# Optimization experiments

Measured on AMD Instinct MI355X. Metric: run time of the kernel, lower is better.

The kernel has to match this reference:

```python
import jax, jax.numpy as jnp
import numpy as np

B, N, E, H = 64, 512, 1024, 16
DH = E // H


def setup_inputs() -> dict:
    key = jax.random.key(0)
    ks = jax.random.split(key, 5)
    x = jax.random.normal(ks[0], (B, N, E), dtype=jnp.float32)
    # Linear weights stored as [in, out] (transpose of torch's [out, in]); y = x @ W + b
    Wqkv = jax.random.normal(ks[1], (E, 3 * E), dtype=jnp.float32) * 0.02
    bqkv = jnp.zeros((3 * E,), dtype=jnp.float32)
    Wproj = jax.random.normal(ks[2], (E, E), dtype=jnp.float32) * 0.02
    bproj = jnp.zeros((E,), dtype=jnp.float32)
    adj = jax.random.randint(ks[3], (N, N), 0, 2, dtype=jnp.int32)
    return {"x": x, "Wqkv": Wqkv, "bqkv": bqkv, "Wproj": Wproj, "bproj": bproj, "adj": adj}


def reference(x, Wqkv, bqkv, Wproj, bproj, adj):
    b, n, e = x.shape
    h, dh = H, e // H
    # fused QKV projection
    qkv = (x @ Wqkv + bqkv).reshape(b, n, 3, h, dh)
    qkv = jnp.transpose(qkv, (2, 0, 3, 1, 4))  # [3, B, H, N, Dh]
    q, k, v = qkv[0], qkv[1], qkv[2]
    # adjacency mask with self-loops (adj + eye, then bool), broadcast over B, H
    mask = (adj + jnp.eye(n, dtype=adj.dtype)) > 0  # [N, N]
    scale = 1.0 / jnp.sqrt(jnp.asarray(dh, dtype=x.dtype))
    scores = jnp.einsum("bhnd,bhmd->bhnm", q, k) * scale  # [B, H, N, N]
    scores = jnp.where(mask[None, None], scores, jnp.finfo(scores.dtype).min)
    attn = jax.nn.softmax(scores, axis=-1)
    y = jnp.einsum("bhnm,bhmd->bhnd", attn, v)  # [B, H, N, Dh]
    y = jnp.transpose(y, (0, 2, 1, 3)).reshape(b, n, e)
    return y @ Wproj + bproj
```

## Files before the change

### kernel.cpp

```cpp
#include <hip/hip_runtime.h>
#include <hip/hip_bf16.h>

#define Bz 64
#define Nz 512
#define Ez 1024
#define Hz 16
#define DHz 64

static constexpr int MROWS = Bz * Nz;
static constexpr int NQKV  = 3 * Ez;

typedef __attribute__((ext_vector_type(8))) short bf16x8_t;
typedef __attribute__((ext_vector_type(4))) float f32x4_t;
typedef __attribute__((ext_vector_type(16))) float f32x16_t;
typedef __attribute__((ext_vector_type(4))) unsigned u32x4_t;

union FragU { bf16x8_t h; u32x4_t u; };

__device__ __forceinline__ unsigned short f2bf(float f) {
    union { float f; unsigned u; } v; v.f = f;
    unsigned r = v.u + 0x7FFFu + ((v.u >> 16) & 1u);
    return (unsigned short)(r >> 16);
}
__device__ __forceinline__ float bf2f(unsigned short h) {
    union { unsigned u; float f; } v; v.u = ((unsigned)h) << 16;
    return v.f;
}
__device__ __forceinline__ unsigned packbf(float a, float b) {
    union { float f; unsigned u; } x, y; x.f = a; y.f = b;
    return ((x.u + 0x8000u) >> 16) | ((y.u + 0x8000u) & 0xFFFF0000u);
}

__device__ __forceinline__ void async16(const unsigned short* g, unsigned short* l) {
    __builtin_amdgcn_global_load_lds(
        (const __attribute__((address_space(1))) void*)g,
        (__attribute__((address_space(3))) void*)l, 16, 0, 0);
}

__device__ __forceinline__ void barrier_lds() {
    asm volatile("s_waitcnt lgkmcnt(0)" ::: "memory");
    __builtin_amdgcn_sched_barrier(0);
    __builtin_amdgcn_s_barrier();
    __builtin_amdgcn_sched_barrier(0);
}

__global__ void cvt_f32_bf16(const float* __restrict__ in,
                             unsigned short* __restrict__ out, int n4) {
    int id = blockIdx.x * blockDim.x + threadIdx.x;
    int stride = gridDim.x * blockDim.x;
    for (int i = id; i < n4; i += stride) {
        float4 f = ((const float4*)in)[i];
        ushort4 o;
        o.x = f2bf(f.x); o.y = f2bf(f.y); o.z = f2bf(f.z); o.w = f2bf(f.w);
        ((ushort4*)out)[i] = o;
    }
}

__global__ __launch_bounds__(256)
void cvt_transpose(const float* __restrict__ in,
                   unsigned short* __restrict__ out,
                   int K, int Ncols) {
    int n  = blockIdx.x * 256 + threadIdx.x;
    int k0 = blockIdx.y * 8;
    bf16x8_t o;
#pragma unroll
    for (int j = 0; j < 8; j++)
        o[j] = (short)f2bf(in[(long)(k0 + j) * Ncols + n]);
    *(bf16x8_t*)&out[(long)n * K + k0] = o;
}

__global__ void build_adjm(const int* __restrict__ adj,
                           unsigned long long* __restrict__ adjm) {
    int id = blockIdx.x * blockDim.x + threadIdx.x;
    int n = id >> 3, w = id & 7;
    const int4* r4 = (const int4*)(adj + (long)n * Nz + w * 64);
    unsigned long long m = 0;
#pragma unroll
    for (int c = 0; c < 16; c++) {
        int4 v = r4[c];
        unsigned long long bits =
            (unsigned long long)(v.x != 0) | ((unsigned long long)(v.y != 0) << 1) |
            ((unsigned long long)(v.z != 0) << 2) | ((unsigned long long)(v.w != 0) << 3);
        m |= bits << (c * 4);
    }
    if ((n >> 6) == w) m |= 1ull << (n & 63);
    adjm[id] = m;
}

template<bool OUT_BF16>
__global__ __launch_bounds__(512, 2)
void gemm_mfma(const unsigned short* __restrict__ A,
               const unsigned short* __restrict__ BT,
               const float* __restrict__ bias,
               void* __restrict__ C,
               int M, int Ncols, int K) {
    const int tid  = threadIdx.x;
    const int w    = tid >> 6;
    const int lane = tid & 63;
    const int m32  = lane & 31;
    const int kh   = lane >> 5;
    const int wm   = (w >> 2) * 128;
    const int wn   = (w & 3) * 64;

    const int nwg = gridDim.x * gridDim.y;
    const int bid = blockIdx.y * gridDim.x + blockIdx.x;
    const int swz = (bid & 7) * (nwg >> 3) + (bid >> 3);
    const int rowBase = (swz / gridDim.x) * 256;
    const int colBase = (swz % gridDim.x) * 256;

    __shared__ __align__(16) unsigned short Abuf[2][256][64];
    __shared__ __align__(16) unsigned short Bbuf[2][256][64];

    f32x16_t acc[4][2];
#pragma unroll
    for (int mi = 0; mi < 4; mi++)
#pragma unroll
        for (int n = 0; n < 2; n++)
#pragma unroll
            for (int r = 0; r < 16; r++)
                acc[mi][n][r] = 0.0f;

    const unsigned short* srcA[4];
    const unsigned short* srcB[4];
#pragma unroll
    for (int li = 0; li < 4; li++) {
        int s = (w * 4 + li) * 64 + lane;
        int r = s >> 3;
        int c = (s & 7) ^ (r & 7);
        srcA[li] = A  + (size_t)(rowBase + r) * K + c * 8;
        srcB[li] = BT + (size_t)(colBase + r) * K + c * 8;
    }
    const int dstOff = w * 2048;

    const int nt = K >> 6;
    const int fsw = m32 & 7;

#pragma unroll
    for (int li = 0; li < 4; li++)
        async16(srcA[li], (unsigned short*)Abuf[0] + dstOff + li * 512);
#pragma unroll
    for (int li = 0; li < 4; li++)
        async16(srcB[li], (unsigned short*)Bbuf[0] + dstOff + li * 512);
#pragma unroll
    for (int li = 0; li < 4; li++)
        async16(srcB[li] + 64, (unsigned short*)Bbuf[1] + dstOff + li * 512);
    asm volatile("s_waitcnt vmcnt(4)" ::: "memory");
    __builtin_amdgcn_sched_barrier(0);
    __builtin_amdgcn_s_barrier();
    __builtin_amdgcn_sched_barrier(0);

    for (int t = 0; t < nt; t++) {
        const int buf = t & 1;
        bf16x8_t af[2][4], bfr[2][4];

        if (t + 1 < nt) {
#pragma unroll
            for (int li = 0; li < 4; li++)
                async16(srcA[li] + (t + 1) * 64,
                        (unsigned short*)Abuf[buf ^ 1] + dstOff + li * 512);
        }
#pragma unroll
        for (int kc = 0; kc < 4; kc++) {
            int p = (kc * 2 + kh) ^ fsw;
#pragma unroll
            for (int n = 0; n < 2; n++)
                bfr[n][kc] = *(const bf16x8_t*)&Bbuf[buf][wn + n * 32 + m32][p * 8];
#pragma unroll
            for (int mi = 0; mi < 2; mi++)
                af[mi][kc] = *(const bf16x8_t*)&Abuf[buf][wm + mi * 32 + m32][p * 8];
        }
        __builtin_amdgcn_s_setprio(1);
#pragma unroll
        for (int kc = 0; kc < 4; kc++)
#pragma unroll
            for (int mi = 0; mi < 2; mi++)
#pragma unroll
                for (int n = 0; n < 2; n++)
                    acc[mi][n] = __builtin_amdgcn_mfma_f32_32x32x16_bf16(
                        af[mi][kc], bfr[n][kc], acc[mi][n], 0, 0, 0);
        __builtin_amdgcn_s_setprio(0);
        barrier_lds();

        if (t + 2 < nt) {
#pragma unroll
            for (int li = 0; li < 4; li++)
                async16(srcB[li] + (t + 2) * 64,
                        (unsigned short*)Bbuf[buf] + dstOff + li * 512);
        }
#pragma unroll
        for (int kc = 0; kc < 4; kc++) {
            int p = (kc * 2 + kh) ^ fsw;
#pragma unroll
            for (int mi = 0; mi < 2; mi++)
                af[mi][kc] = *(const bf16x8_t*)&Abuf[buf][wm + 64 + mi * 32 + m32][p * 8];
        }
        __builtin_amdgcn_s_setprio(1);
#pragma unroll
        for (int kc = 0; kc < 4; kc++)
#pragma unroll
            for (int mi = 0; mi < 2; mi++)
#pragma unroll
                for (int n = 0; n < 2; n++)
                    acc[2 + mi][n] = __builtin_amdgcn_mfma_f32_32x32x16_bf16(
                        af[mi][kc], bfr[n][kc], acc[2 + mi][n], 0, 0, 0);
        __builtin_amdgcn_s_setprio(0);

        if (t + 2 < nt) {
            asm volatile("s_waitcnt vmcnt(4)" ::: "memory");
            barrier_lds();
        } else if (t + 1 < nt) {
            asm volatile("s_waitcnt vmcnt(0)" ::: "memory");
            barrier_lds();
        }
    }

#pragma unroll
    for (int n = 0; n < 2; n++) {
        int col = colBase + wn + n * 32 + m32;
        float bv = bias[col];
#pragma unroll
        for (int mi = 0; mi < 4; mi++) {
#pragma unroll
            for (int reg = 0; reg < 16; reg++) {
                int row = rowBase + wm + mi * 32 + (reg & 3) + 8 * (reg >> 2) + 4 * kh;
                float v = acc[mi][n][reg] + bv;
                if (OUT_BF16)
                    ((unsigned short*)C)[(size_t)row * Ncols + col] = f2bf(v);
                else
                    ((float*)C)[(size_t)row * Ncols + col] = v;
            }
        }
    }
}

__global__ __launch_bounds__(512, 2)
void attn_mfma(const unsigned short* __restrict__ qkv,
               const unsigned long long* __restrict__ adjm,
               unsigned short* __restrict__ y)
{
    const int h = blockIdx.x;
    const int b = blockIdx.y;
    const int tid  = threadIdx.x;
    const int lane = tid & 63;
    const int w    = tid >> 6;
    const int l16  = lane & 15;
    const int q    = lane >> 4;

    __shared__ __align__(16) unsigned short Ks[512][64];
    __shared__ __align__(16) unsigned short Vt[64][512];

    const long rowB = (long)b * Nz;
    const unsigned short* base = qkv + rowB * NQKV;

    for (int idx = tid; idx < 4096; idx += 512) {
        int n = idx >> 3, cc = idx & 7;
        *(bf16x8_t*)&Ks[n][(cc ^ (n & 7)) * 8] =
            *(const bf16x8_t*)&base[(long)n * NQKV + Ez + h * DHz + cc * 8];
    }
    {
        int tp = tid & 255, dh = tid >> 8;
        int n0 = tp * 2;
        bf16x8_t va[4], vb[4];
#pragma unroll
        for (int c = 0; c < 4; c++) {
            va[c] = *(const bf16x8_t*)&base[(long)n0 * NQKV + 2 * Ez + h * DHz + dh * 32 + c * 8];
            vb[c] = *(const bf16x8_t*)&base[(long)(n0 + 1) * NQKV + 2 * Ez + h * DHz + dh * 32 + c * 8];
        }
        unsigned short* vt = &Vt[0][0];
#pragma unroll
        for (int dd = 0; dd < 32; dd++) {
            int d = dh * 32 + dd;
            unsigned lo = (unsigned)(unsigned short)va[dd >> 3][dd & 7];
            unsigned hi = (unsigned)(unsigned short)vb[dd >> 3][dd & 7];
            int cp = (n0 >> 3) ^ (d & 7);
            *(unsigned*)&vt[d * 512 + cp * 8 + (n0 & 7)] = lo | (hi << 16);
        }
    }
    FragU qf[4][2];
#pragma unroll
    for (int mt = 0; mt < 4; mt++)
#pragma unroll
        for (int kc = 0; kc < 2; kc++)
            qf[mt][kc].h = *(const bf16x8_t*)&base[(long)(w * 64 + mt * 16 + l16) * NQKV
                                                   + h * DHz + kc * 32 + q * 8];
    __syncthreads();

    f32x4_t oacc[4][4];
#pragma unroll
    for (int mt = 0; mt < 4; mt++)
#pragma unroll
        for (int dt = 0; dt < 4; dt++) {
            f32x4_t z = {0.0f, 0.0f, 0.0f, 0.0f};
            oacc[mt][dt] = z;
        }
    float rsum[4] = {0.0f, 0.0f, 0.0f, 0.0f};
    unsigned long long wm[4];

    for (int ct = 0; ct < 16; ct++) {
        const int j0 = ct * 32;
        if ((ct & 1) == 0) {
#pragma unroll
            for (int mt = 0; mt < 4; mt++)
                wm[mt] = adjm[(size_t)(w * 64 + mt * 16 + l16) * 8 + (ct >> 1)];
        }
        bf16x8_t kf[2][2];
#pragma unroll
        for (int jt = 0; jt < 2; jt++)
#pragma unroll
            for (int kc = 0; kc < 2; kc++)
                kf[jt][kc] = *(const bf16x8_t*)
                    &Ks[j0 + jt * 16 + l16][((kc * 4 + q) ^ (l16 & 7)) * 8];

        f32x4_t tacc[2][4];
#pragma unroll
        for (int jt = 0; jt < 2; jt++)
#pragma unroll
            for (int mt = 0; mt < 4; mt++) {
                f32x4_t z = {0.0f, 0.0f, 0.0f, 0.0f};
                z = __builtin_amdgcn_mfma_f32_16x16x32_bf16(kf[jt][0], qf[mt][0].h, z, 0, 0, 0);
                tacc[jt][mt] = __builtin_amdgcn_mfma_f32_16x16x32_bf16(kf[jt][1], qf[mt][1].h, z, 0, 0, 0);
            }

        unsigned pk[2][4][2];
#pragma unroll
        for (int jt = 0; jt < 2; jt++)
#pragma unroll
            for (int mt = 0; mt < 4; mt++) {
                float e[4];
#pragma unroll
                for (int r = 0; r < 4; r++) {
                    int jrel = (ct & 1) * 32 + jt * 16 + q * 4 + r;
                    bool bit = (wm[mt] >> jrel) & 1ull;
                    float ev = bit ? __expf(tacc[jt][mt][r] * 0.125f) : 0.0f;
                    e[r] = ev;
                    rsum[mt] += ev;
                }
                pk[jt][mt][0] = packbf(e[0], e[1]);
                pk[jt][mt][1] = packbf(e[2], e[3]);
            }

        bf16x8_t vf[4];
#pragma unroll
        for (int dt = 0; dt < 4; dt++) {
            int d = dt * 16 + l16;
            int cp = (ct * 4 + q) ^ (l16 & 7);
            vf[dt] = *(const bf16x8_t*)&(&Vt[0][0])[d * 512 + cp * 8];
        }

#pragma unroll
        for (int mt = 0; mt < 4; mt++) {
            FragU pf;
#pragma unroll
            for (int p = 0; p < 4; p++) {
                int srcl = ((lane & 16) << 1) | ((p & 2) << 3) | l16;
                unsigned a0 = (unsigned)__shfl((int)pk[0][mt][p & 1], srcl);
                unsigned a1 = (unsigned)__shfl((int)pk[1][mt][p & 1], srcl);
                pf.u[p] = (lane & 32) ? a1 : a0;
            }
#pragma unroll
            for (int dt = 0; dt < 4; dt++)
                oacc[mt][dt] = __builtin_amdgcn_mfma_f32_16x16x32_bf16(
                    pf.h, vf[dt], oacc[mt][dt], 0, 0, 0);
        }
    }

#pragma unroll
    for (int mt = 0; mt < 4; mt++) {
        float s = rsum[mt];
        s += __shfl_xor(s, 16);
        s += __shfl_xor(s, 32);
#pragma unroll
        for (int r = 0; r < 4; r++) {
            float rs = __shfl(s, (lane & 48) | (q * 4) | r);
            float inv = 1.0f / rs;
            int row = w * 64 + mt * 16 + q * 4 + r;
#pragma unroll
            for (int dt = 0; dt < 4; dt++)
                y[(rowB + row) * Ez + h * DHz + dt * 16 + l16] =
                    f2bf(oacc[mt][dt][r] * inv);
        }
    }
}

extern "C" void kernel_launch(void* const* d_in, const int* in_sizes, int n_in,
                              void* d_out, int out_size, void* d_ws, size_t ws_size,
                              hipStream_t stream) {
    const float* x     = (const float*)d_in[0];
    const float* Wqkv  = (const float*)d_in[1];
    const float* bqkv  = (const float*)d_in[2];
    const float* Wproj = (const float*)d_in[3];
    const float* bproj = (const float*)d_in[4];
    const int*   adj   = (const int*)d_in[5];
    float* out = (float*)d_out;

    char* ws = (char*)d_ws;
    unsigned short* xb     = (unsigned short*)(ws);
    unsigned short* qkv    = (unsigned short*)(ws + 67108864);
    unsigned short* WqkvT  = (unsigned short*)(ws + 268435456);
    unsigned short* WprojT = (unsigned short*)(ws + 274726912);
    unsigned long long* adjm = (unsigned long long*)(ws + 276824064);
    unsigned short* yb = xb;

    cvt_f32_bf16<<<8192, 256, 0, stream>>>(x, xb, (Bz * Nz * Ez) / 4);
    cvt_transpose<<<dim3(NQKV / 256, Ez / 8), 256, 0, stream>>>(Wqkv, WqkvT, Ez, NQKV);
    cvt_transpose<<<dim3(Ez / 256, Ez / 8), 256, 0, stream>>>(Wproj, WprojT, Ez, Ez);
    build_adjm<<<16, 256, 0, stream>>>(adj, adjm);

    gemm_mfma<true><<<dim3(NQKV / 256, MROWS / 256), 512, 0, stream>>>(
        xb, WqkvT, bqkv, qkv, MROWS, NQKV, Ez);

    attn_mfma<<<dim3(Hz, Bz), 512, 0, stream>>>(qkv, adjm, yb);

    gemm_mfma<false><<<dim3(Ez / 256, MROWS / 256), 512, 0, stream>>>(
        yb, WprojT, bproj, out, MROWS, Ez, Ez);
}
```

Measured before the change: 753.5 us.

## Restructure GEMM main loop into four half-K phases with finer async staging

Splits each 64-wide K tile of the bf16 GEMM into two 32-wide halves stored in separate LDS buffers, packing two logical rows per 64-element LDS row with a new XOR swizzle. The main loop becomes four phases, each issuing one async global-to-LDS stage, reading fragments and running eight MFMAs between barriers. The aim is to spread global loads more evenly across the iteration and keep more loads in flight, hiding memory latency behind MFMA work. In exchange it adds more barriers per tile and intricate vmcnt bookkeeping that must match the load count exactly.

```diff
diff --git a/kernel.cpp b/kernel.cpp
--- a/kernel.cpp
+++ b/kernel.cpp
@@ -37,12 +37,7 @@
         (__attribute__((address_space(3))) void*)l, 16, 0, 0);
 }
 
-__device__ __forceinline__ void barrier_lds() {
-    asm volatile("s_waitcnt lgkmcnt(0)" ::: "memory");
-    __builtin_amdgcn_sched_barrier(0);
-    __builtin_amdgcn_s_barrier();
-    __builtin_amdgcn_sched_barrier(0);
-}
+#define MFMA32(a, b, c) __builtin_amdgcn_mfma_f32_32x32x16_bf16(a, b, c, 0, 0, 0)
 
 __global__ void cvt_f32_bf16(const float* __restrict__ in,
                              unsigned short* __restrict__ out, int n4) {
@@ -108,8 +103,8 @@
     const int rowBase = (swz / gridDim.x) * 256;
     const int colBase = (swz % gridDim.x) * 256;
 
-    __shared__ __align__(16) unsigned short Abuf[2][256][64];
-    __shared__ __align__(16) unsigned short Bbuf[2][256][64];
+    __shared__ __align__(16) unsigned short Ah[2][2][128][64];
+    __shared__ __align__(16) unsigned short Bh[2][2][128][64];
 
     f32x16_t acc[4][2];
 #pragma unroll
@@ -120,99 +115,112 @@
             for (int r = 0; r < 16; r++)
                 acc[mi][n][r] = 0.0f;
 
-    const unsigned short* srcA[4];
-    const unsigned short* srcB[4];
-#pragma unroll
-    for (int li = 0; li < 4; li++) {
-        int s = (w * 4 + li) * 64 + lane;
-        int r = s >> 3;
-        int c = (s & 7) ^ (r & 7);
-        srcA[li] = A  + (size_t)(rowBase + r) * K + c * 8;
-        srcB[li] = BT + (size_t)(colBase + r) * K + c * 8;
-    }
-    const int dstOff = w * 2048;
+    const unsigned short* sA[2];
+    const unsigned short* sB[2];
+#pragma unroll
+    for (int l = 0; l < 2; l++) {
+        int s = l * 512 + tid;
+        int R = s >> 3, g = s & 7;
+        int lg = g ^ (R & 7);
+        int grow = 2 * R + (lg >> 2);
+        int gc8 = (lg & 3) * 8;
+        sA[l] = A  + (size_t)(rowBase + grow) * K + gc8;
+        sB[l] = BT + (size_t)(colBase + grow) * K + gc8;
+    }
+    const int dst0 = w * 512;
+
+#define STAGE(src, dst, tt, half) do {                                   \
+        unsigned short* d_ = &(dst)[0][0];                               \
+        async16((src)[0] + (size_t)(tt) * 64 + (half) * 32, d_ + dst0);  \
+        async16((src)[1] + (size_t)(tt) * 64 + (half) * 32, d_ + 4096 + dst0); \
+    } while (0)
+
+    const int Ra  = wm / 2 + (m32 >> 1);
+    const int Rb  = wn / 2 + (m32 >> 1);
+    const int key = (m32 >> 1) & 7;
+    const int lgb = (m32 & 1) * 4 + kh;
 
     const int nt = K >> 6;
-    const int fsw = m32 & 7;
-
-#pragma unroll
-    for (int li = 0; li < 4; li++)
-        async16(srcA[li], (unsigned short*)Abuf[0] + dstOff + li * 512);
-#pragma unroll
-    for (int li = 0; li < 4; li++)
-        async16(srcB[li], (unsigned short*)Bbuf[0] + dstOff + li * 512);
-#pragma unroll
-    for (int li = 0; li < 4; li++)
-        async16(srcB[li] + 64, (unsigned short*)Bbuf[1] + dstOff + li * 512);
-    asm volatile("s_waitcnt vmcnt(4)" ::: "memory");
+
+    STAGE(sA, Ah[0][0], 0, 0);
+    STAGE(sB, Bh[0][0], 0, 0);
+    STAGE(sA, Ah[0][1], 0, 1);
+    STAGE(sB, Bh[0][1], 0, 1);
+    STAGE(sA, Ah[1][0], 1, 0);
+    STAGE(sB, Bh[1][0], 1, 0);
+    asm volatile("s_waitcnt vmcnt(8)" ::: "memory");
     __builtin_amdgcn_sched_barrier(0);
     __builtin_amdgcn_s_barrier();
     __builtin_amdgcn_sched_barrier(0);
 
-    for (int t = 0; t < nt; t++) {
+    for (int t = 0; t < nt; ++t) {
         const int buf = t & 1;
-        bf16x8_t af[2][4], bfr[2][4];
-
-        if (t + 1 < nt) {
-#pragma unroll
-            for (int li = 0; li < 4; li++)
-                async16(srcA[li] + (t + 1) * 64,
-                        (unsigned short*)Abuf[buf ^ 1] + dstOff + li * 512);
-        }
-#pragma unroll
-        for (int kc = 0; kc < 4; kc++) {
-            int p = (kc * 2 + kh) ^ fsw;
-#pragma unroll
-            for (int n = 0; n < 2; n++)
-                bfr[n][kc] = *(const bf16x8_t*)&Bbuf[buf][wn + n * 32 + m32][p * 8];
-#pragma unroll
-            for (int mi = 0; mi < 2; mi++)
-                af[mi][kc] = *(const bf16x8_t*)&Abuf[buf][wm + mi * 32 + m32][p * 8];
-        }
-        __builtin_amdgcn_s_setprio(1);
-#pragma unroll
-        for (int kc = 0; kc < 4; kc++)
-#pragma unroll
-            for (int mi = 0; mi < 2; mi++)
-#pragma unroll
-                for (int n = 0; n < 2; n++)
-                    acc[mi][n] = __builtin_amdgcn_mfma_f32_32x32x16_bf16(
-                        af[mi][kc], bfr[n][kc], acc[mi][n], 0, 0, 0);
-        __builtin_amdgcn_s_setprio(0);
-        barrier_lds();
-
-        if (t + 2 < nt) {
-#pragma unroll
-            for (int li = 0; li < 4; li++)
-                async16(srcB[li] + (t + 2) * 64,
-                        (unsigned short*)Bbuf[buf] + dstOff + li * 512);
-        }
-#pragma unroll
-        for (int kc = 0; kc < 4; kc++) {
-            int p = (kc * 2 + kh) ^ fsw;
-#pragma unroll
-            for (int mi = 0; mi < 2; mi++)
-                af[mi][kc] = *(const bf16x8_t*)&Abuf[buf][wm + 64 + mi * 32 + m32][p * 8];
-        }
-        __builtin_amdgcn_s_setprio(1);
-#pragma unroll
-        for (int kc = 0; kc < 4; kc++)
-#pragma unroll
-            for (int mi = 0; mi < 2; mi++)
-#pragma unroll
-                for (int n = 0; n < 2; n++)
-                    acc[2 + mi][n] = __builtin_amdgcn_mfma_f32_32x32x16_bf16(
-                        af[mi][kc], bfr[n][kc], acc[2 + mi][n], 0, 0, 0);
-        __builtin_amdgcn_s_setprio(0);
-
-        if (t + 2 < nt) {
-            asm volatile("s_waitcnt vmcnt(4)" ::: "memory");
-            barrier_lds();
-        } else if (t + 1 < nt) {
-            asm volatile("s_waitcnt vmcnt(0)" ::: "memory");
-            barrier_lds();
-        }
-    }
+        const unsigned short *Ab, *Bb;
+        bf16x8_t a0, a1, a2, a3, b0, b1;
+        int gp8;
+
+#define PHASE_READS()                                                    \
+        a0 = *(const bf16x8_t*)(Ab + (Ra +  0) * 64 + gp8);              \
+        a1 = *(const bf16x8_t*)(Ab + (Ra + 16) * 64 + gp8);              \
+        a2 = *(const bf16x8_t*)(Ab + (Ra + 32) * 64 + gp8);              \
+        a3 = *(const bf16x8_t*)(Ab + (Ra + 48) * 64 + gp8);              \
+        b0 = *(const bf16x8_t*)(Bb + (Rb +  0) * 64 + gp8);              \
+        b1 = *(const bf16x8_t*)(Bb + (Rb + 16) * 64 + gp8)
+
+#define PHASE_MFMA()                                                     \
+        __builtin_amdgcn_s_barrier();                                    \
+        asm volatile("s_waitcnt lgkmcnt(0)" ::: "memory");               \
+        __builtin_amdgcn_sched_barrier(0);                               \
+        __builtin_amdgcn_s_setprio(1);                                   \
+        acc[0][0] = MFMA32(a0, b0, acc[0][0]);                           \
+        acc[0][1] = MFMA32(a0, b1, acc[0][1]);                           \
+        acc[1][0] = MFMA32(a1, b0, acc[1][0]);                           \
+        acc[1][1] = MFMA32(a1, b1, acc[1][1]);                           \
+        acc[2][0] = MFMA32(a2, b0, acc[2][0]);                           \
+        acc[2][1] = MFMA32(a2, b1, acc[2][1]);                           \
+        acc[3][0] = MFMA32(a3, b0, acc[3][0]);                           \
+        acc[3][1] = MFMA32(a3, b1, acc[3][1]);                           \
+        __builtin_amdgcn_s_setprio(0)
+
+#define PHASE_CLOSE()                                                    \
+        __builtin_amdgcn_sched_barrier(0);                               \
+        __builtin_amdgcn_s_barrier();                                    \
+        __builtin_amdgcn_sched_barrier(0)
+
+        Ab = &Ah[buf][0][0][0]; Bb = &Bh[buf][0][0][0];
+        gp8 = ((lgb + 0) ^ key) * 8;
+        PHASE_READS();
+        if (t + 1 < nt) STAGE(sA, Ah[buf ^ 1][1], t + 1, 1);
+        PHASE_MFMA();
+        PHASE_CLOSE();
+
+        gp8 = ((lgb + 2) ^ key) * 8;
+        PHASE_READS();
+        if (t + 1 < nt) STAGE(sB, Bh[buf ^ 1][1], t + 1, 1);
+        PHASE_MFMA();
+        if (t < nt - 1) { asm volatile("s_waitcnt vmcnt(8)" ::: "memory"); }
+        else            { asm volatile("s_waitcnt vmcnt(0)" ::: "memory"); }
+        PHASE_CLOSE();
+
+        Ab = &Ah[buf][1][0][0]; Bb = &Bh[buf][1][0][0];
+        gp8 = ((lgb + 0) ^ key) * 8;
+        PHASE_READS();
+        if (t + 2 < nt) STAGE(sA, Ah[buf][0], t + 2, 0);
+        PHASE_MFMA();
+        PHASE_CLOSE();
+
+        gp8 = ((lgb + 2) ^ key) * 8;
+        PHASE_READS();
+        if (t + 2 < nt) STAGE(sB, Bh[buf][0], t + 2, 0);
+        PHASE_MFMA();
+        if (t < nt - 2)       { asm volatile("s_waitcnt vmcnt(8)" ::: "memory"); }
+        else if (t == nt - 2) { asm volatile("s_waitcnt vmcnt(4)" ::: "memory"); }
+        PHASE_CLOSE();
+    }
+#undef PHASE_READS
+#undef PHASE_MFMA
+#undef PHASE_CLOSE
+#undef STAGE
 
 #pragma unroll
     for (int n = 0; n < 2; n++) {
```

After: 743.3 us. About the same (-1.4%).
